# Performance work log

Measured on AMD Instinct MI355X. Metric: run time of the kernel, lower is better.

Reference implementation:

```python
import jax, jax.numpy as jnp
import numpy as np

EMBED_DIM = 10
CHEB_K = 2
DIM_IN = 64
DIM_OUT = 64
BATCH = 64
NUM_NODES = 4096


def setup_inputs() -> dict:
    key = jax.random.key(0)
    k1, k2, k3 = jax.random.split(key, 3)
    x = jax.random.normal(k1, (BATCH, NUM_NODES, DIM_IN), dtype=jnp.float32)
    node_embeddings = jax.random.normal(k2, (NUM_NODES, EMBED_DIM), dtype=jnp.float32)
    # xavier-uniform-like init for weights_pool, zeros for bias_pool
    fan_in = EMBED_DIM * CHEB_K * DIM_IN
    fan_out = DIM_OUT
    limit = float(np.sqrt(6.0 / (fan_in + fan_out)))
    weights_pool = jax.random.uniform(k3, (EMBED_DIM, CHEB_K, DIM_IN, DIM_OUT), dtype=jnp.float32, minval=-limit, maxval=limit)
    bias_pool = jnp.zeros((EMBED_DIM, DIM_OUT), dtype=jnp.float32)
    return {"x": x, "node_embeddings": node_embeddings, "weights_pool": weights_pool, "bias_pool": bias_pool}


def reference(x, node_embeddings, weights_pool, bias_pool):
    num_nodes = x.shape[1]
    # adaptive support: softmax(relu(E E^T)) over last dim  [N, N]
    sim = jax.nn.relu(node_embeddings @ node_embeddings.T)
    supports1 = jax.nn.softmax(sim, axis=-1)
    eye = jnp.eye(num_nodes, dtype=x.dtype)
    supports = jnp.stack([eye, supports1], axis=0)  # [k, N, N]
    # per-node weights and bias from node embeddings
    weights = jnp.einsum('nd,dkio->nkio', node_embeddings, weights_pool)  # [N, k, Ci, Co]
    bias = node_embeddings @ bias_pool  # [N, Co]
    # graph diffusion: [k, N, M] x [B, M, Ci] -> [B, N, k, Ci]
    x_g = jnp.einsum('knm,bmc->bnkc', supports, x)
    # per-node GEMM: [B, N, k, Ci] x [N, k, Ci, Co] -> [B, N, Co]
    x_gconv = jnp.einsum('bnki,nkio->bno', x_g, weights) + bias
    return x_gconv
```

## Files before the change

### kernel.cpp

```cpp
#include <hip/hip_runtime.h>
#include <cstdint>
#include <cstddef>

#define N_NODES 4096
#define EMB 10
#define BATCH_SZ 64
#define CI 64
#define CO 64
#define LKP 136

#define BM 256
#define BN 128
#define SLOT_U16 24576
#define BOFF_U16 16384

typedef unsigned short u16;
typedef __bf16 bf16x8 __attribute__((ext_vector_type(8)));
typedef float f32x4 __attribute__((ext_vector_type(4)));

__device__ __forceinline__ u16 f2bf(float f) {
  union { float f; uint32_t u; } v; v.f = f;
  const uint32_t r = v.u + 0x7fffu + ((v.u >> 16) & 1u);
  return (u16)(r >> 16);
}

__device__ __forceinline__ void gload16(const void* g, void* l) {
  __builtin_amdgcn_global_load_lds(
      (__attribute__((address_space(1))) void*)(g),
      (__attribute__((address_space(3))) void*)(l), 16, 0, 0);
}

__global__ __launch_bounds__(256) void support_softmax(
    const float* __restrict__ E, u16* __restrict__ Sb) {
  __shared__ float sim[4][N_NODES];
  __shared__ float EnS[4][EMB];
  __shared__ float red[4][4];
  const int n0 = blockIdx.x * 4;
  const int t = threadIdx.x;
  const int wid = t >> 6;
  if (t < 4 * EMB) EnS[t / EMB][t % EMB] = E[n0 * EMB + t];
  __syncthreads();
  float en[4][EMB];
#pragma unroll
  for (int r = 0; r < 4; ++r)
#pragma unroll
    for (int d = 0; d < EMB; ++d) en[r][d] = EnS[r][d];

  float rmax[4] = {-1e30f, -1e30f, -1e30f, -1e30f};
  for (int p = 0; p < 16; ++p) {
    const int m = p * 256 + t;
    const float2* e2 = reinterpret_cast<const float2*>(E + m * EMB);
    float em[EMB];
    const float2 v0 = e2[0], v1 = e2[1], v2 = e2[2], v3 = e2[3], v4 = e2[4];
    em[0] = v0.x; em[1] = v0.y; em[2] = v1.x; em[3] = v1.y; em[4] = v2.x;
    em[5] = v2.y; em[6] = v3.x; em[7] = v3.y; em[8] = v4.x; em[9] = v4.y;
#pragma unroll
    for (int r = 0; r < 4; ++r) {
      float acc = 0.f;
#pragma unroll
      for (int d = 0; d < EMB; ++d) acc += en[r][d] * em[d];
      acc = fmaxf(acc, 0.f);
      sim[r][m] = acc;
      rmax[r] = fmaxf(rmax[r], acc);
    }
  }
#pragma unroll
  for (int r = 0; r < 4; ++r) {
#pragma unroll
    for (int s = 32; s; s >>= 1) rmax[r] = fmaxf(rmax[r], __shfl_xor(rmax[r], s));
  }
  if ((t & 63) == 0) {
#pragma unroll
    for (int r = 0; r < 4; ++r) red[r][wid] = rmax[r];
  }
  __syncthreads();
  float gmax[4];
#pragma unroll
  for (int r = 0; r < 4; ++r)
    gmax[r] = fmaxf(fmaxf(red[r][0], red[r][1]), fmaxf(red[r][2], red[r][3]));
  __syncthreads();

  float rsum[4] = {0.f, 0.f, 0.f, 0.f};
  for (int p = 0; p < 16; ++p) {
    const int m = p * 256 + t;
#pragma unroll
    for (int r = 0; r < 4; ++r) {
      const float e = __expf(sim[r][m] - gmax[r]);
      sim[r][m] = e;
      rsum[r] += e;
    }
  }
#pragma unroll
  for (int r = 0; r < 4; ++r) {
#pragma unroll
    for (int s = 32; s; s >>= 1) rsum[r] += __shfl_xor(rsum[r], s);
  }
  if ((t & 63) == 0) {
#pragma unroll
    for (int r = 0; r < 4; ++r) red[r][wid] = rsum[r];
  }
  __syncthreads();
  float inv[4];
#pragma unroll
  for (int r = 0; r < 4; ++r)
    inv[r] = 1.0f / (red[r][0] + red[r][1] + red[r][2] + red[r][3]);

  for (int p = 0; p < 16; ++p) {
    const int m = p * 256 + t;
#pragma unroll
    for (int r = 0; r < 4; ++r)
      Sb[(size_t)(n0 + r) * N_NODES + m] = f2bf(sim[r][m] * inv[r]);
  }
}

__global__ __launch_bounds__(256) void convert_x(
    const float* __restrict__ x, u16* __restrict__ Xt) {
  __shared__ float sm[64][65];
  const int b = blockIdx.x, mt = blockIdx.y;
  const int t = threadIdx.x;
  const int c = t & 63, q = t >> 6;
  const float* xp = x + ((size_t)b * N_NODES + mt * 64) * CI;
#pragma unroll
  for (int p = 0; p < 16; ++p) {
    const int r = q + p * 4;
    sm[r][c] = xp[(size_t)r * CI + c];
  }
  __syncthreads();
  u16* op = Xt + (size_t)(b * 64) * N_NODES + mt * 64;
#pragma unroll
  for (int p = 0; p < 16; ++p) {
    const int cc = q + p * 4;
    op[(size_t)cc * N_NODES + c] = f2bf(sm[c][cc]);
  }
}

__global__ __launch_bounds__(512) void diffuse_gemm_pipe(
    const u16* __restrict__ S, const u16* __restrict__ Xt,
    u16* __restrict__ Zb) {
  __shared__ __align__(16) u16 lds[3 * SLOT_U16];
  const int tid = threadIdx.x;
  const int lane = tid & 63;
  const int w = tid >> 6;
  const int bid = blockIdx.x;
  const int sw = (bid & 7) * 64 + (bid >> 3);
  const int by = sw >> 5;
  const int bx = sw & 31;
  const int n0 = by * BM;
  const int j0 = bx * BN;

  const int lrow8 = lane >> 3;
  const int scol = 8 * ((lane & 7) ^ lrow8);
  const u16* gsrc[6];
  const u16* lbase[6];
#pragma unroll
  for (int i = 0; i < 6; ++i) {
    const int chunk = w * 6 + i;
    if (chunk < 32) {
      const int row = chunk * 8 + lrow8;
      gsrc[i] = S + (size_t)(n0 + row) * N_NODES + scol;
      lbase[i] = &lds[chunk * 512];
    } else {
      const int row = (chunk - 32) * 8 + lrow8;
      gsrc[i] = Xt + (size_t)(j0 + row) * N_NODES + scol;
      lbase[i] = &lds[BOFF_U16 + (chunk - 32) * 512];
    }
  }

  const int wm = w >> 1, wn = w & 1;
  const int fr = lane & 15;
  const int khalf = lane >> 4;
  const int swz16 = (fr & 7) << 3;

  f32x4 acc[4][4];
#pragma unroll
  for (int i = 0; i < 4; ++i)
#pragma unroll
    for (int j = 0; j < 4; ++j) acc[i][j] = (f32x4)0.f;

#define STAGE(tt)                                                         \
  {                                                                       \
    const int _s = (tt) % 3;                                              \
    _Pragma("unroll")                                                     \
    for (int i = 0; i < 6; ++i)                                           \
      gload16(gsrc[i] + (size_t)(tt) * 64,                                \
              (void*)(lbase[i] + _s * SLOT_U16));                         \
  }

#define COMPUTE(ss)                                                       \
  {                                                                       \
    const u16* sa = &lds[(ss) * SLOT_U16];                                \
    const u16* sb = sa + BOFF_U16;                                        \
    _Pragma("unroll")                                                     \
    for (int ks = 0; ks < 2; ++ks) {                                      \
      const int c16 = (ks * 32 + khalf * 8) ^ swz16;                      \
      bf16x8 a[4], b[4];                                                  \
      _Pragma("unroll")                                                   \
      for (int fm = 0; fm < 4; ++fm)                                      \
        a[fm] = *reinterpret_cast<const bf16x8*>(                         \
            &sa[(wm * 64 + fm * 16 + fr) * 64 + c16]);                    \
      _Pragma("unroll")                                                   \
      for (int fn = 0; fn < 4; ++fn)                                      \
        b[fn] = *reinterpret_cast<const bf16x8*>(                         \
            &sb[(wn * 64 + fn * 16 + fr) * 64 + c16]);                    \
      __builtin_amdgcn_s_setprio(1);                                      \
      _Pragma("unroll")                                                   \
      for (int fm = 0; fm < 4; ++fm)                                      \
        _Pragma("unroll")                                                 \
        for (int fn = 0; fn < 4; ++fn)                                    \
          acc[fm][fn] = __builtin_amdgcn_mfma_f32_16x16x32_bf16(          \
              a[fm], b[fn], acc[fm][fn], 0, 0, 0);                        \
      __builtin_amdgcn_s_setprio(0);                                      \
    }                                                                     \
  }

  STAGE(0);
  STAGE(1);

  int s = 0;
  for (int t = 0; t < 62; ++t) {
    asm volatile("s_waitcnt vmcnt(6)" ::: "memory");
    __builtin_amdgcn_s_barrier();
    __builtin_amdgcn_sched_barrier(0);
    STAGE(t + 2);
    COMPUTE(s);
    s = (s == 2) ? 0 : s + 1;
  }
  asm volatile("s_waitcnt vmcnt(6)" ::: "memory");
  __builtin_amdgcn_s_barrier();
  __builtin_amdgcn_sched_barrier(0);
  COMPUTE(s);
  s = (s == 2) ? 0 : s + 1;
  asm volatile("s_waitcnt vmcnt(0)" ::: "memory");
  __builtin_amdgcn_s_barrier();
  __builtin_amdgcn_sched_barrier(0);
  COMPUTE(s);

  const int crow = (lane >> 4) * 4;
  const int ccol = lane & 15;
#pragma unroll
  for (int fm = 0; fm < 4; ++fm) {
    const int nrow = n0 + wm * 64 + fm * 16 + crow;
#pragma unroll
    for (int fn = 0; fn < 4; ++fn) {
      const int jcol = j0 + wn * 64 + fn * 16 + ccol;
#pragma unroll
      for (int r = 0; r < 4; ++r)
        Zb[(size_t)(nrow + r) * N_NODES + jcol] = f2bf(acc[fm][fn][r]);
    }
  }
#undef STAGE
#undef COMPUTE
}

__global__ __launch_bounds__(256) void node_gemm_mfma(
    const float* __restrict__ x, const u16* __restrict__ Zb,
    const float* __restrict__ E, const float* __restrict__ wp,
    const float* __restrict__ bp, float* __restrict__ out) {
  __shared__ __align__(16) u16 Wt[2][64][LKP];
  __shared__ __align__(16) u16 Axz[2][64][LKP];
  __shared__ float biasS[2][64];
  __shared__ float EnS[2][EMB];
  const int n0 = blockIdx.x * 2;
  const int t = threadIdx.x;
  const int lane = t & 63;
  const int w = t >> 6;
  if (t < 2 * EMB) EnS[t / EMB][t % EMB] = E[n0 * EMB + t];
  __syncthreads();
  float en0[EMB], en1[EMB];
#pragma unroll
  for (int d = 0; d < EMB; ++d) { en0[d] = EnS[0][d]; en1[d] = EnS[1][d]; }

  if (t < 128) {
    const int nn = t >> 6, o = t & 63;
    float b = 0.f;
#pragma unroll
    for (int d = 0; d < EMB; ++d) b += EnS[nn][d] * bp[d * CO + o];
    biasS[nn][o] = b;
  }

  const float4* wp4 = reinterpret_cast<const float4*>(wp);
#pragma unroll
  for (int p = 0; p < 8; ++p) {
    const int e4 = p * 256 + t;
    const int ki = e4 >> 4, o4 = e4 & 15;
    float a0x = 0.f, a0y = 0.f, a0z = 0.f, a0w = 0.f;
    float a1x = 0.f, a1y = 0.f, a1z = 0.f, a1w = 0.f;
#pragma unroll
    for (int d = 0; d < EMB; ++d) {
      const float4 wv = wp4[d * 2048 + e4];
      a0x += en0[d] * wv.x; a0y += en0[d] * wv.y;
      a0z += en0[d] * wv.z; a0w += en0[d] * wv.w;
      a1x += en1[d] * wv.x; a1y += en1[d] * wv.y;
      a1z += en1[d] * wv.z; a1w += en1[d] * wv.w;
    }
    Wt[0][o4 * 4 + 0][ki] = f2bf(a0x); Wt[0][o4 * 4 + 1][ki] = f2bf(a0y);
    Wt[0][o4 * 4 + 2][ki] = f2bf(a0z); Wt[0][o4 * 4 + 3][ki] = f2bf(a0w);
    Wt[1][o4 * 4 + 0][ki] = f2bf(a1x); Wt[1][o4 * 4 + 1][ki] = f2bf(a1y);
    Wt[1][o4 * 4 + 2][ki] = f2bf(a1z); Wt[1][o4 * 4 + 3][ki] = f2bf(a1w);
  }

#pragma unroll
  for (int nn = 0; nn < 2; ++nn) {
    const int ng = n0 + nn;
#pragma unroll
    for (int pb = 0; pb < 4; ++pb) {
      const int b = pb * 16 + (t >> 4);
      const int i0 = (t & 15) * 4;
      const float4 xv = *reinterpret_cast<const float4*>(
          &x[(size_t)b * (N_NODES * CI) + (size_t)ng * CI + i0]);
      ushort4 uv;
      uv.x = f2bf(xv.x); uv.y = f2bf(xv.y); uv.z = f2bf(xv.z); uv.w = f2bf(xv.w);
      *reinterpret_cast<ushort4*>(&Axz[nn][b][i0]) = uv;
    }
#pragma unroll
    for (int pz = 0; pz < 4; ++pz) {
      const int t4 = pz * 256 + t;
      const int b = t4 >> 4, c0 = (t4 & 15) * 4;
      const ushort4 zv = *reinterpret_cast<const ushort4*>(
          &Zb[(size_t)ng * N_NODES + t4 * 4]);
      *reinterpret_cast<ushort4*>(&Axz[nn][b][64 + c0]) = zv;
    }
  }
  __syncthreads();

  const int nn = w >> 1, bh = w & 1;
  const int fr = lane & 15, fk = (lane >> 4) * 8;
  f32x4 acc[2][4];
#pragma unroll
  for (int m = 0; m < 2; ++m)
#pragma unroll
    for (int n = 0; n < 4; ++n) acc[m][n] = (f32x4)0.f;

#pragma unroll
  for (int kk = 0; kk < 4; ++kk) {
    bf16x8 a[2], b[4];
#pragma unroll
    for (int m = 0; m < 2; ++m)
      a[m] = *reinterpret_cast<const bf16x8*>(
          &Axz[nn][bh * 32 + m * 16 + fr][kk * 32 + fk]);
#pragma unroll
    for (int n = 0; n < 4; ++n)
      b[n] = *reinterpret_cast<const bf16x8*>(
          &Wt[nn][n * 16 + fr][kk * 32 + fk]);
#pragma unroll
    for (int m = 0; m < 2; ++m)
#pragma unroll
      for (int n = 0; n < 4; ++n)
        acc[m][n] = __builtin_amdgcn_mfma_f32_16x16x32_bf16(
            a[m], b[n], acc[m][n], 0, 0, 0);
  }

  const int crow = (lane >> 4) * 4;
  const int ccol = lane & 15;
  const int ng = n0 + nn;
#pragma unroll
  for (int m = 0; m < 2; ++m) {
#pragma unroll
    for (int n = 0; n < 4; ++n) {
      const int o = n * 16 + ccol;
      const float bv = biasS[nn][o];
#pragma unroll
      for (int r = 0; r < 4; ++r) {
        const int b = bh * 32 + m * 16 + crow + r;
        out[(size_t)b * (N_NODES * CI) + (size_t)ng * CI + o] =
            acc[m][n][r] + bv;
      }
    }
  }
}

extern "C" void kernel_launch(void* const* d_in, const int* in_sizes, int n_in,
                              void* d_out, int out_size, void* d_ws, size_t ws_size,
                              hipStream_t stream) {
  const float* x  = (const float*)d_in[0];
  const float* E  = (const float*)d_in[1];
  const float* wp = (const float*)d_in[2];
  const float* bp = (const float*)d_in[3];
  float* out = (float*)d_out;
  const size_t MAT = (size_t)N_NODES * N_NODES;
  u16* Sb = (u16*)d_ws;
  u16* Xt = Sb + MAT;
  u16* Zb = Xt + MAT;

  support_softmax<<<N_NODES / 4, 256, 0, stream>>>(E, Sb);
  convert_x<<<dim3(BATCH_SZ, N_NODES / 64), 256, 0, stream>>>(x, Xt);
  diffuse_gemm_pipe<<<512, 512, 0, stream>>>(Sb, Xt, Zb);
  node_gemm_mfma<<<N_NODES / 2, 256, 0, stream>>>(x, Zb, E, wp, bp, out);
}
```

Baseline: 322.8 us.

## Precompute per-node bf16 weights in a separate kernel and remap GEMM tiles per XCD

Adds a wgen kernel that builds all per-node bf16 weight matrices at once, reusing weights_pool loads across 64 nodes, and writes them into the workspace over the now-dead S buffer. node_gemm_mfma then loads these precomputed weights instead of recomputing the embedding-weighted sum with repeated weights_pool reads per block. The diffusion GEMM block-to-tile mapping is also changed so each XCD covers a compact 8x8 tile region, which should improve L2 locality. The cost is an extra launch and about 64MB of extra global traffic for the weight buffer.

```diff
diff --git a/kernel.cpp b/kernel.cpp
--- a/kernel.cpp
+++ b/kernel.cpp
@@ -142,9 +142,10 @@
   const int lane = tid & 63;
   const int w = tid >> 6;
   const int bid = blockIdx.x;
-  const int sw = (bid & 7) * 64 + (bid >> 3);
-  const int by = sw >> 5;
-  const int bx = sw & 31;
+  const int xcd = bid & 7;
+  const int inner = bid >> 3;
+  const int by = (xcd >> 2) * 8 + (inner >> 4) * 2 + (inner & 1);
+  const int bx = (xcd & 3) * 8 + ((inner >> 1) & 7);
   const int n0 = by * BM;
   const int j0 = bx * BN;
 
@@ -252,9 +253,47 @@
 #undef COMPUTE
 }
 
+__global__ __launch_bounds__(256) void wgen(
+    const float* __restrict__ E, const float* __restrict__ wp,
+    u16* __restrict__ Wall) {
+  __shared__ float en_s[64][EMB];
+  const int n0 = blockIdx.x * 64;
+  const int t = threadIdx.x;
+#pragma unroll
+  for (int p = 0; p < 3; ++p) {
+    const int idx = p * 256 + t;
+    if (idx < 64 * EMB) en_s[idx / EMB][idx % EMB] = E[n0 * EMB + idx];
+  }
+  __syncthreads();
+
+  const float4* wp4 = reinterpret_cast<const float4*>(wp);
+#pragma unroll
+  for (int it = 0; it < 8; ++it) {
+    const int slot = it * 256 + t;
+    const int ki = slot >> 4, o4 = slot & 15;
+    float4 wv[EMB];
+#pragma unroll
+    for (int d = 0; d < EMB; ++d) wv[d] = wp4[d * 2048 + slot];
+#pragma unroll 8
+    for (int n = 0; n < 64; ++n) {
+      float ax = 0.f, ay = 0.f, az = 0.f, aw = 0.f;
+#pragma unroll
+      for (int d = 0; d < EMB; ++d) {
+        const float e = en_s[n][d];
+        ax += e * wv[d].x; ay += e * wv[d].y;
+        az += e * wv[d].z; aw += e * wv[d].w;
+      }
+      ushort4 uv;
+      uv.x = f2bf(ax); uv.y = f2bf(ay); uv.z = f2bf(az); uv.w = f2bf(aw);
+      *reinterpret_cast<ushort4*>(
+          &Wall[((size_t)(n0 + n) * 128 + ki) * 64 + o4 * 4]) = uv;
+    }
+  }
+}
+
 __global__ __launch_bounds__(256) void node_gemm_mfma(
     const float* __restrict__ x, const u16* __restrict__ Zb,
-    const float* __restrict__ E, const float* __restrict__ wp,
+    const u16* __restrict__ Wall, const float* __restrict__ E,
     const float* __restrict__ bp, float* __restrict__ out) {
   __shared__ __align__(16) u16 Wt[2][64][LKP];
   __shared__ __align__(16) u16 Axz[2][64][LKP];
@@ -266,9 +305,6 @@
   const int w = t >> 6;
   if (t < 2 * EMB) EnS[t / EMB][t % EMB] = E[n0 * EMB + t];
   __syncthreads();
-  float en0[EMB], en1[EMB];
-#pragma unroll
-  for (int d = 0; d < EMB; ++d) { en0[d] = EnS[0][d]; en1[d] = EnS[1][d]; }
 
   if (t < 128) {
     const int nn = t >> 6, o = t & 63;
@@ -278,25 +314,20 @@
     biasS[nn][o] = b;
   }
 
-  const float4* wp4 = reinterpret_cast<const float4*>(wp);
-#pragma unroll
-  for (int p = 0; p < 8; ++p) {
-    const int e4 = p * 256 + t;
-    const int ki = e4 >> 4, o4 = e4 & 15;
-    float a0x = 0.f, a0y = 0.f, a0z = 0.f, a0w = 0.f;
-    float a1x = 0.f, a1y = 0.f, a1z = 0.f, a1w = 0.f;
-#pragma unroll
-    for (int d = 0; d < EMB; ++d) {
-      const float4 wv = wp4[d * 2048 + e4];
-      a0x += en0[d] * wv.x; a0y += en0[d] * wv.y;
-      a0z += en0[d] * wv.z; a0w += en0[d] * wv.w;
-      a1x += en1[d] * wv.x; a1y += en1[d] * wv.y;
-      a1z += en1[d] * wv.z; a1w += en1[d] * wv.w;
-    }
-    Wt[0][o4 * 4 + 0][ki] = f2bf(a0x); Wt[0][o4 * 4 + 1][ki] = f2bf(a0y);
-    Wt[0][o4 * 4 + 2][ki] = f2bf(a0z); Wt[0][o4 * 4 + 3][ki] = f2bf(a0w);
-    Wt[1][o4 * 4 + 0][ki] = f2bf(a1x); Wt[1][o4 * 4 + 1][ki] = f2bf(a1y);
-    Wt[1][o4 * 4 + 2][ki] = f2bf(a1z); Wt[1][o4 * 4 + 3][ki] = f2bf(a1w);
+#pragma unroll
+  for (int nn = 0; nn < 2; ++nn) {
+    const u16* wsrc = Wall + (size_t)(n0 + nn) * 8192;
+#pragma unroll
+    for (int p = 0; p < 4; ++p) {
+      const int slot = p * 256 + t;
+      const int ki = slot >> 3, o8 = slot & 7;
+      const ushort4 v0 = *reinterpret_cast<const ushort4*>(&wsrc[ki * 64 + o8 * 8]);
+      const ushort4 v1 = *reinterpret_cast<const ushort4*>(&wsrc[ki * 64 + o8 * 8 + 4]);
+      Wt[nn][o8 * 8 + 0][ki] = v0.x; Wt[nn][o8 * 8 + 1][ki] = v0.y;
+      Wt[nn][o8 * 8 + 2][ki] = v0.z; Wt[nn][o8 * 8 + 3][ki] = v0.w;
+      Wt[nn][o8 * 8 + 4][ki] = v1.x; Wt[nn][o8 * 8 + 5][ki] = v1.y;
+      Wt[nn][o8 * 8 + 6][ki] = v1.z; Wt[nn][o8 * 8 + 7][ki] = v1.w;
+    }
   }
 
 #pragma unroll
@@ -381,9 +412,11 @@
   u16* Sb = (u16*)d_ws;
   u16* Xt = Sb + MAT;
   u16* Zb = Xt + MAT;
+  u16* Wall = (u16*)d_ws;
 
   support_softmax<<<N_NODES / 4, 256, 0, stream>>>(E, Sb);
   convert_x<<<dim3(BATCH_SZ, N_NODES / 64), 256, 0, stream>>>(x, Xt);
   diffuse_gemm_pipe<<<512, 512, 0, stream>>>(Sb, Xt, Zb);
-  node_gemm_mfma<<<N_NODES / 2, 256, 0, stream>>>(x, Zb, E, wp, bp, out);
-}
+  wgen<<<N_NODES / 64, 256, 0, stream>>>(E, wp, Wall);
+  node_gemm_mfma<<<N_NODES / 2, 256, 0, stream>>>(x, Zb, Wall, E, bp, out);
+}
```

After: 372.2 us. 1.15x slower.

## Fuse front kernels, split GEMM k-loop into interleaved phases, remap tiles per XCD

Applied to the files above, without the earlier changes.

Merges the softmax-support kernel and the x transpose/convert kernel into one launch with block-index dispatch, which removes a launch and lets the two run concurrently. The main diffusion GEMM now splits each k-tile into two phases that each issue half of the next stage's async loads between LDS fragment reads and MFMAs, with extra barriers. Block-to-tile mapping is changed so each XCD covers a compact 2D region of tiles, aiming for better L2 reuse. The risks are more barriers per iteration and the larger shared-memory footprint of the fused kernel, which could lower occupancy for the convert blocks.

```diff
diff --git a/kernel.cpp b/kernel.cpp
--- a/kernel.cpp
+++ b/kernel.cpp
@@ -30,107 +30,108 @@
       (__attribute__((address_space(3))) void*)(l), 16, 0, 0);
 }
 
-__global__ __launch_bounds__(256) void support_softmax(
-    const float* __restrict__ E, u16* __restrict__ Sb) {
-  __shared__ float sim[4][N_NODES];
+__global__ __launch_bounds__(256) void front_fused(
+    const float* __restrict__ E, const float* __restrict__ x,
+    u16* __restrict__ Sb, u16* __restrict__ Xt) {
+  __shared__ float sbuf[4][N_NODES];
   __shared__ float EnS[4][EMB];
   __shared__ float red[4][4];
-  const int n0 = blockIdx.x * 4;
   const int t = threadIdx.x;
-  const int wid = t >> 6;
-  if (t < 4 * EMB) EnS[t / EMB][t % EMB] = E[n0 * EMB + t];
-  __syncthreads();
-  float en[4][EMB];
-#pragma unroll
-  for (int r = 0; r < 4; ++r)
-#pragma unroll
-    for (int d = 0; d < EMB; ++d) en[r][d] = EnS[r][d];
-
-  float rmax[4] = {-1e30f, -1e30f, -1e30f, -1e30f};
-  for (int p = 0; p < 16; ++p) {
-    const int m = p * 256 + t;
-    const float2* e2 = reinterpret_cast<const float2*>(E + m * EMB);
-    float em[EMB];
-    const float2 v0 = e2[0], v1 = e2[1], v2 = e2[2], v3 = e2[3], v4 = e2[4];
-    em[0] = v0.x; em[1] = v0.y; em[2] = v1.x; em[3] = v1.y; em[4] = v2.x;
-    em[5] = v2.y; em[6] = v3.x; em[7] = v3.y; em[8] = v4.x; em[9] = v4.y;
+
+  if (blockIdx.x < 1024) {
+    const int n0 = blockIdx.x * 4;
+    const int wid = t >> 6;
+    if (t < 4 * EMB) EnS[t / EMB][t % EMB] = E[n0 * EMB + t];
+    __syncthreads();
+    float en[4][EMB];
+#pragma unroll
+    for (int r = 0; r < 4; ++r)
+#pragma unroll
+      for (int d = 0; d < EMB; ++d) en[r][d] = EnS[r][d];
+
+    float rmax[4] = {-1e30f, -1e30f, -1e30f, -1e30f};
+    for (int p = 0; p < 16; ++p) {
+      const int m = p * 256 + t;
+      const float2* e2 = reinterpret_cast<const float2*>(E + m * EMB);
+      float em[EMB];
+      const float2 v0 = e2[0], v1 = e2[1], v2 = e2[2], v3 = e2[3], v4 = e2[4];
+      em[0] = v0.x; em[1] = v0.y; em[2] = v1.x; em[3] = v1.y; em[4] = v2.x;
+      em[5] = v2.y; em[6] = v3.x; em[7] = v3.y; em[8] = v4.x; em[9] = v4.y;
+#pragma unroll
+      for (int r = 0; r < 4; ++r) {
+        float acc = 0.f;
+#pragma unroll
+        for (int d = 0; d < EMB; ++d) acc += en[r][d] * em[d];
+        acc = fmaxf(acc, 0.f);
+        sbuf[r][m] = acc;
+        rmax[r] = fmaxf(rmax[r], acc);
+      }
+    }
 #pragma unroll
     for (int r = 0; r < 4; ++r) {
-      float acc = 0.f;
-#pragma unroll
-      for (int d = 0; d < EMB; ++d) acc += en[r][d] * em[d];
-      acc = fmaxf(acc, 0.f);
-      sim[r][m] = acc;
-      rmax[r] = fmaxf(rmax[r], acc);
-    }
-  }
-#pragma unroll
-  for (int r = 0; r < 4; ++r) {
-#pragma unroll
-    for (int s = 32; s; s >>= 1) rmax[r] = fmaxf(rmax[r], __shfl_xor(rmax[r], s));
-  }
-  if ((t & 63) == 0) {
-#pragma unroll
-    for (int r = 0; r < 4; ++r) red[r][wid] = rmax[r];
-  }
-  __syncthreads();
-  float gmax[4];
-#pragma unroll
-  for (int r = 0; r < 4; ++r)
-    gmax[r] = fmaxf(fmaxf(red[r][0], red[r][1]), fmaxf(red[r][2], red[r][3]));
-  __syncthreads();
-
-  float rsum[4] = {0.f, 0.f, 0.f, 0.f};
-  for (int p = 0; p < 16; ++p) {
-    const int m = p * 256 + t;
+#pragma unroll
+      for (int s = 32; s; s >>= 1) rmax[r] = fmaxf(rmax[r], __shfl_xor(rmax[r], s));
+    }
+    if ((t & 63) == 0) {
+#pragma unroll
+      for (int r = 0; r < 4; ++r) red[r][wid] = rmax[r];
+    }
+    __syncthreads();
+    float gmax[4];
+#pragma unroll
+    for (int r = 0; r < 4; ++r)
+      gmax[r] = fmaxf(fmaxf(red[r][0], red[r][1]), fmaxf(red[r][2], red[r][3]));
+    __syncthreads();
+
+    float rsum[4] = {0.f, 0.f, 0.f, 0.f};
+    for (int p = 0; p < 16; ++p) {
+      const int m = p * 256 + t;
+#pragma unroll
+      for (int r = 0; r < 4; ++r) {
+        const float e = __expf(sbuf[r][m] - gmax[r]);
+        sbuf[r][m] = e;
+        rsum[r] += e;
+      }
+    }
 #pragma unroll
     for (int r = 0; r < 4; ++r) {
-      const float e = __expf(sim[r][m] - gmax[r]);
-      sim[r][m] = e;
-      rsum[r] += e;
-    }
-  }
-#pragma unroll
-  for (int r = 0; r < 4; ++r) {
-#pragma unroll
-    for (int s = 32; s; s >>= 1) rsum[r] += __shfl_xor(rsum[r], s);
-  }
-  if ((t & 63) == 0) {
-#pragma unroll
-    for (int r = 0; r < 4; ++r) red[r][wid] = rsum[r];
-  }
-  __syncthreads();
-  float inv[4];
-#pragma unroll
-  for (int r = 0; r < 4; ++r)
-    inv[r] = 1.0f / (red[r][0] + red[r][1] + red[r][2] + red[r][3]);
-
-  for (int p = 0; p < 16; ++p) {
-    const int m = p * 256 + t;
+#pragma unroll
+      for (int s = 32; s; s >>= 1) rsum[r] += __shfl_xor(rsum[r], s);
+    }
+    if ((t & 63) == 0) {
+#pragma unroll
+      for (int r = 0; r < 4; ++r) red[r][wid] = rsum[r];
+    }
+    __syncthreads();
+    float inv[4];
 #pragma unroll
     for (int r = 0; r < 4; ++r)
-      Sb[(size_t)(n0 + r) * N_NODES + m] = f2bf(sim[r][m] * inv[r]);
-  }
-}
-
-__global__ __launch_bounds__(256) void convert_x(
-    const float* __restrict__ x, u16* __restrict__ Xt) {
-  __shared__ float sm[64][65];
-  const int b = blockIdx.x, mt = blockIdx.y;
-  const int t = threadIdx.x;
-  const int c = t & 63, q = t >> 6;
-  const float* xp = x + ((size_t)b * N_NODES + mt * 64) * CI;
-#pragma unroll
-  for (int p = 0; p < 16; ++p) {
-    const int r = q + p * 4;
-    sm[r][c] = xp[(size_t)r * CI + c];
-  }
-  __syncthreads();
-  u16* op = Xt + (size_t)(b * 64) * N_NODES + mt * 64;
-#pragma unroll
-  for (int p = 0; p < 16; ++p) {
-    const int cc = q + p * 4;
-    op[(size_t)cc * N_NODES + c] = f2bf(sm[c][cc]);
+      inv[r] = 1.0f / (red[r][0] + red[r][1] + red[r][2] + red[r][3]);
+
+    for (int p = 0; p < 16; ++p) {
+      const int m = p * 256 + t;
+#pragma unroll
+      for (int r = 0; r < 4; ++r)
+        Sb[(size_t)(n0 + r) * N_NODES + m] = f2bf(sbuf[r][m] * inv[r]);
+    }
+  } else {
+    const int idx = blockIdx.x - 1024;
+    const int b = idx & 63, mt = idx >> 6;
+    float (*sm)[65] = reinterpret_cast<float (*)[65]>(&sbuf[0][0]);
+    const int c = t & 63, q = t >> 6;
+    const float* xp = x + ((size_t)b * N_NODES + mt * 64) * CI;
+#pragma unroll
+    for (int p = 0; p < 16; ++p) {
+      const int r = q + p * 4;
+      sm[r][c] = xp[(size_t)r * CI + c];
+    }
+    __syncthreads();
+    u16* op = Xt + (size_t)(b * 64) * N_NODES + mt * 64;
+#pragma unroll
+    for (int p = 0; p < 16; ++p) {
+      const int cc = q + p * 4;
+      op[(size_t)cc * N_NODES + c] = f2bf(sm[c][cc]);
+    }
   }
 }
 
@@ -142,9 +143,10 @@
   const int lane = tid & 63;
   const int w = tid >> 6;
   const int bid = blockIdx.x;
-  const int sw = (bid & 7) * 64 + (bid >> 3);
-  const int by = sw >> 5;
-  const int bx = sw & 31;
+  const int xcd = bid & 7;
+  const int inner = bid >> 3;
+  const int by = (xcd >> 2) * 8 + (inner >> 4) * 2 + (inner & 1);
+  const int bx = (xcd & 3) * 8 + ((inner >> 1) & 7);
   const int n0 = by * BM;
   const int j0 = bx * BN;
 
@@ -177,63 +179,66 @@
 #pragma unroll
     for (int j = 0; j < 4; ++j) acc[i][j] = (f32x4)0.f;
 
-#define STAGE(tt)                                                         \
+#define STAGE3(tt, h)                                                     \
   {                                                                       \
     const int _s = (tt) % 3;                                              \
     _Pragma("unroll")                                                     \
-    for (int i = 0; i < 6; ++i)                                           \
+    for (int i = (h) * 3; i < (h) * 3 + 3; ++i)                           \
       gload16(gsrc[i] + (size_t)(tt) * 64,                                \
               (void*)(lbase[i] + _s * SLOT_U16));                         \
   }
 
-#define COMPUTE(ss)                                                       \
+#define PHASE(ksv, dostage, tt, h)                                        \
   {                                                                       \
-    const u16* sa = &lds[(ss) * SLOT_U16];                                \
+    const u16* sa = &lds[s * SLOT_U16];                                   \
     const u16* sb = sa + BOFF_U16;                                        \
+    const int c16 = ((ksv) * 32 + khalf * 8) ^ swz16;                     \
+    bf16x8 a[4], b[4];                                                    \
     _Pragma("unroll")                                                     \
-    for (int ks = 0; ks < 2; ++ks) {                                      \
-      const int c16 = (ks * 32 + khalf * 8) ^ swz16;                      \
-      bf16x8 a[4], b[4];                                                  \
-      _Pragma("unroll")                                                   \
-      for (int fm = 0; fm < 4; ++fm)                                      \
-        a[fm] = *reinterpret_cast<const bf16x8*>(                         \
-            &sa[(wm * 64 + fm * 16 + fr) * 64 + c16]);                    \
+    for (int fm = 0; fm < 4; ++fm)                                        \
+      a[fm] = *reinterpret_cast<const bf16x8*>(                           \
+          &sa[(wm * 64 + fm * 16 + fr) * 64 + c16]);                      \
+    _Pragma("unroll")                                                     \
+    for (int fn = 0; fn < 4; ++fn)                                        \
+      b[fn] = *reinterpret_cast<const bf16x8*>(                           \
+          &sb[(wn * 64 + fn * 16 + fr) * 64 + c16]);                      \
+    if (dostage) STAGE3(tt, h);                                           \
+    __builtin_amdgcn_s_barrier();                                         \
+    asm volatile("s_waitcnt lgkmcnt(0)" ::: "memory");                    \
+    __builtin_amdgcn_sched_barrier(0);                                    \
+    __builtin_amdgcn_s_setprio(1);                                        \
+    _Pragma("unroll")                                                     \
+    for (int fm = 0; fm < 4; ++fm)                                        \
       _Pragma("unroll")                                                   \
       for (int fn = 0; fn < 4; ++fn)                                      \
-        b[fn] = *reinterpret_cast<const bf16x8*>(                         \
-            &sb[(wn * 64 + fn * 16 + fr) * 64 + c16]);                    \
-      __builtin_amdgcn_s_setprio(1);                                      \
-      _Pragma("unroll")                                                   \
-      for (int fm = 0; fm < 4; ++fm)                                      \
-        _Pragma("unroll")                                                 \
-        for (int fn = 0; fn < 4; ++fn)                                    \
-          acc[fm][fn] = __builtin_amdgcn_mfma_f32_16x16x32_bf16(          \
-              a[fm], b[fn], acc[fm][fn], 0, 0, 0);                        \
-      __builtin_amdgcn_s_setprio(0);                                      \
-    }                                                                     \
-  }
-
-  STAGE(0);
-  STAGE(1);
+        acc[fm][fn] = __builtin_amdgcn_mfma_f32_16x16x32_bf16(            \
+            a[fm], b[fn], acc[fm][fn], 0, 0, 0);                          \
+    __builtin_amdgcn_s_setprio(0);                                        \
+  }
+
+  STAGE3(0, 0); STAGE3(0, 1);
+  STAGE3(1, 0); STAGE3(1, 1);
 
   int s = 0;
   for (int t = 0; t < 62; ++t) {
     asm volatile("s_waitcnt vmcnt(6)" ::: "memory");
     __builtin_amdgcn_s_barrier();
-    __builtin_amdgcn_sched_barrier(0);
-    STAGE(t + 2);
-    COMPUTE(s);
+    PHASE(0, true, t + 2, 0);
+    __builtin_amdgcn_s_barrier();
+    PHASE(1, true, t + 2, 1);
     s = (s == 2) ? 0 : s + 1;
   }
   asm volatile("s_waitcnt vmcnt(6)" ::: "memory");
   __builtin_amdgcn_s_barrier();
-  __builtin_amdgcn_sched_barrier(0);
-  COMPUTE(s);
+  PHASE(0, false, 0, 0);
+  __builtin_amdgcn_s_barrier();
+  PHASE(1, false, 0, 0);
   s = (s == 2) ? 0 : s + 1;
   asm volatile("s_waitcnt vmcnt(0)" ::: "memory");
   __builtin_amdgcn_s_barrier();
-  __builtin_amdgcn_sched_barrier(0);
-  COMPUTE(s);
+  PHASE(0, false, 0, 0);
+  __builtin_amdgcn_s_barrier();
+  PHASE(1, false, 0, 0);
 
   const int crow = (lane >> 4) * 4;
   const int ccol = lane & 15;
@@ -248,8 +253,8 @@
         Zb[(size_t)(nrow + r) * N_NODES + jcol] = f2bf(acc[fm][fn][r]);
     }
   }
-#undef STAGE
-#undef COMPUTE
+#undef STAGE3
+#undef PHASE
 }
 
 __global__ __launch_bounds__(256) void node_gemm_mfma(
@@ -382,8 +387,7 @@
   u16* Xt = Sb + MAT;
   u16* Zb = Xt + MAT;
 
-  support_softmax<<<N_NODES / 4, 256, 0, stream>>>(E, Sb);
-  convert_x<<<dim3(BATCH_SZ, N_NODES / 64), 256, 0, stream>>>(x, Xt);
+  front_fused<<<1024 + 4096, 256, 0, stream>>>(E, x, Sb, Xt);
   diffuse_gemm_pipe<<<512, 512, 0, stream>>>(Sb, Xt, Zb);
   node_gemm_mfma<<<N_NODES / 2, 256, 0, stream>>>(x, Zb, E, wp, bp, out);
 }
```

Measured after the change: 308.1 us. -4.6%, faster.
